# Kernel tuning notes

Measured on AMD Instinct MI355X. Metric: run time of the kernel, lower is better.

## Reference

```python
import jax, jax.numpy as jnp
import numpy as np

KH, KW = 2, 2
GRID_SIZE = 5
SPLINE_ORDER = 3
IN_FEATURES = KH * KW
N_COEF = GRID_SIZE + SPLINE_ORDER  # 8
N_KNOTS = GRID_SIZE + 2 * SPLINE_ORDER + 1  # 12


def b_splines(x, grid, spline_order):
    """x: (N, in), grid: (in, n_knots) -> (N, in, grid_size + spline_order).
    Cox-de-Boor recursion, identical to efficient-kan's b_splines."""
    x_ = x[..., None]  # (N, in, 1)
    bases = ((x_ >= grid[:, :-1]) & (x_ < grid[:, 1:])).astype(x.dtype)
    for k in range(1, spline_order + 1):
        left = (x_ - grid[:, : -(k + 1)]) / (grid[:, k:-1] - grid[:, : -(k + 1)])
        right = (grid[:, k + 1:] - x_) / (grid[:, k + 1:] - grid[:, 1:-k])
        bases = left * bases[..., :-1] + right * bases[..., 1:]
    return bases  # (N, in, N_COEF)


def setup_inputs() -> dict:
    key = jax.random.key(0)
    k1, k2, k3, k4 = jax.random.split(key, 4)
    B, C, H, W = 8, 16, 128, 128
    x = jax.random.normal(k1, (B, C, H, W), dtype=jnp.float32) * 0.5  # mostly inside grid_range
    base_weight = jax.random.normal(k2, (1, IN_FEATURES), dtype=jnp.float32) * 0.5
    spline_weight = jax.random.normal(k3, (1, IN_FEATURES, N_COEF), dtype=jnp.float32) * 0.1
    spline_scaler = 1.0 + jax.random.normal(k4, (1, IN_FEATURES), dtype=jnp.float32) * 0.1
    # uniform extended knot grid over grid_range=[-1, 1], same per input feature (buffer)
    h = 2.0 / GRID_SIZE
    g = np.arange(-SPLINE_ORDER, GRID_SIZE + SPLINE_ORDER + 1, dtype=np.float32) * h - 1.0
    grid = jnp.asarray(np.broadcast_to(g, (IN_FEATURES, N_KNOTS)).copy())
    return {"x": x, "base_weight": base_weight, "spline_weight": spline_weight,
            "spline_scaler": spline_scaler, "grid": grid}


def reference(x, base_weight, spline_weight, spline_scaler, grid):
    B, C, H, W = x.shape
    Ho, Wo = H - KH + 1, W - KW + 1  # stride 1, no padding, no dilation
    # unfold: (B, C, Ho, Wo, KH*KW), window elements in torch Unfold row-major order
    patches = jnp.stack([x[:, :, i:i + Ho, j:j + Wo]
                         for i in range(KH) for j in range(KW)], axis=-1)
    flat = patches.reshape(-1, IN_FEATURES)  # (N, 4)
    # KANLinear: base path (SiLU activation then linear)
    base = jax.nn.silu(flat) @ base_weight.T  # (N, 1)
    # spline path
    bas = b_splines(flat, grid, SPLINE_ORDER)  # (N, 4, 8)
    sw = spline_weight * spline_scaler[..., None]  # scaled_spline_weight (1, 4, 8)
    spline = bas.reshape(flat.shape[0], -1) @ sw.reshape(sw.shape[0], -1).T  # (N, 1)
    out = (base + spline).reshape(B, C, Ho, Wo)
    # multiple_convs_kan_conv2d accumulates the per-channel results into one output channel
    return out.sum(axis=1, keepdims=True)  # (B, 1, Ho, Wo)
```

## Files before the change

### kernel.cpp

```cpp
#include <hip/hip_runtime.h>


#define KH 2
#define KW 2
#define IN_F 4
#define N_COEF 8
#define N_INTERVALS 11

__device__ __forceinline__ float silu(float x) {
    return x * __builtin_amdgcn_rcpf(1.0f + __expf(-x));
}

__global__ __launch_bounds__(256) void kan_conv_kernel(
    const float* __restrict__ x,
    const float* __restrict__ base_w,
    const float* __restrict__ spline_w,
    const float* __restrict__ spline_s,
    const float* __restrict__ grid,
    float* __restrict__ out,
    int B, int C, int H, int W)
{
    const int Ho = H - 1, Wo = W - 1;

    __shared__ float4 coef[N_INTERVALS][IN_F];
    __shared__ float s_bw[IN_F];
    __shared__ float s_g0, s_invh;

    const int tid = threadIdx.x;
    if (tid < N_INTERVALS * IN_F) {
        const int t = tid / IN_F;
        const int p = tid % IN_F;
        const float M[4][4] = {
            {1.f/6.f, -3.f/6.f,  3.f/6.f, -1.f/6.f},
            {4.f/6.f,  0.f,     -6.f/6.f,  3.f/6.f},
            {1.f/6.f,  3.f/6.f,  3.f/6.f, -3.f/6.f},
            {0.f,      0.f,      0.f,      1.f/6.f}};
        const float scal = spline_s[p];
        float c0 = 0.f, c1 = 0.f, c2 = 0.f, c3 = 0.f;
        #pragma unroll
        for (int m = 0; m < 4; ++m) {
            const int j = t - 3 + m;
            const float w = (j >= 0 && j < N_COEF)
                              ? spline_w[p * N_COEF + j] * scal : 0.f;
            c0 += M[m][0] * w; c1 += M[m][1] * w;
            c2 += M[m][2] * w; c3 += M[m][3] * w;
        }
        coef[t][p] = make_float4(c0, c1, c2, c3);
    }
    if (tid < IN_F) s_bw[tid] = base_w[tid];
    if (tid == 0) { s_g0 = grid[0]; s_invh = 1.0f / (grid[1] - grid[0]); }
    __syncthreads();

    const float g0 = s_g0, invh = s_invh;
    const float bw0 = s_bw[0], bw1 = s_bw[1], bw2 = s_bw[2], bw3 = s_bw[3];

    const int total = B * Ho * Wo;
    const int HW = H * W;

    for (int o = blockIdx.x * blockDim.x + tid; o < total;
         o += gridDim.x * blockDim.x) {
        const int wo = o % Wo;
        const int rest = o / Wo;
        const int ho = rest % Ho;
        const int b = rest / Ho;

        const float* xb = x + (size_t)b * C * HW + (size_t)ho * W + wo;

        float acc = 0.f;
        #pragma unroll 4
        for (int c = 0; c < 16; ++c) {
            const float* xc = xb + (size_t)c * HW;
            const float v00 = xc[0];
            const float v01 = xc[1];
            const float v10 = xc[W];
            const float v11 = xc[W + 1];

            acc += silu(v00) * bw0 + silu(v01) * bw1 +
                   silu(v10) * bw2 + silu(v11) * bw3;

            #pragma unroll
            for (int p = 0; p < 4; ++p) {
                const float v = (p == 0) ? v00 : (p == 1) ? v01
                              : (p == 2) ? v10 : v11;
                const float tf = (v - g0) * invh;
                const float tfl = floorf(tf);
                const int ti = (int)tfl;
                if ((unsigned)ti < (unsigned)N_INTERVALS) {
                    const float u = tf - tfl;
                    const float4 cf = coef[ti][p];
                    float sp = fmaf(u, cf.w, cf.z);
                    sp = fmaf(u, sp, cf.y);
                    sp = fmaf(u, sp, cf.x);
                    acc += sp;
                }
            }
        }
        out[o] = acc;
    }
}

extern "C" void kernel_launch(void* const* d_in, const int* in_sizes, int n_in,
                              void* d_out, int out_size, void* d_ws, size_t ws_size,
                              hipStream_t stream) {
    const float* x        = (const float*)d_in[0];
    const float* base_w   = (const float*)d_in[1];
    const float* spline_w = (const float*)d_in[2];
    const float* spline_s = (const float*)d_in[3];
    const float* grid     = (const float*)d_in[4];
    float* out = (float*)d_out;

    const int B = 8, C = 16, H = 128, W = 128;
    const int total = B * (H - 1) * (W - 1);
    const int threads = 256;
    const int blocks = (total + threads - 1) / threads;

    kan_conv_kernel<<<blocks, threads, 0, stream>>>(
        x, base_w, spline_w, spline_s, grid, out, B, C, H, W);
}
```

Measured before the change: 75.58 us.

## Tile spatially with shared-memory per-pixel feature reuse and split channels across blocks

```diff
diff --git a/kernel.cpp b/kernel.cpp
--- a/kernel.cpp
+++ b/kernel.cpp
@@ -1,11 +1,15 @@
 #include <hip/hip_runtime.h>
 
 
-#define KH 2
-#define KW 2
 #define IN_F 4
 #define N_COEF 8
-#define N_INTERVALS 11
+#define N_INT 11
+#define TW 32
+#define TH 8
+#define LW 33
+#define LH 9
+#define NV (LW * LH)
+#define CG 4
 
 __device__ __forceinline__ float silu(float x) {
     return x * __builtin_amdgcn_rcpf(1.0f + __expf(-x));
@@ -22,12 +26,13 @@
 {
     const int Ho = H - 1, Wo = W - 1;
 
-    __shared__ float4 coef[N_INTERVALS][IN_F];
-    __shared__ float s_bw[IN_F];
-    __shared__ float s_g0, s_invh;
+    __shared__ float4 coef[N_INT][IN_F];
+    __shared__ float  sfeat[IN_F][NV];
+    __shared__ float  s_misc[6];
 
     const int tid = threadIdx.x;
-    if (tid < N_INTERVALS * IN_F) {
+
+    if (tid < N_INT * IN_F) {
         const int t = tid / IN_F;
         const int p = tid % IN_F;
         const float M[4][4] = {
@@ -47,56 +52,69 @@
         }
         coef[t][p] = make_float4(c0, c1, c2, c3);
     }
-    if (tid < IN_F) s_bw[tid] = base_w[tid];
-    if (tid == 0) { s_g0 = grid[0]; s_invh = 1.0f / (grid[1] - grid[0]); }
+    if (tid < IN_F) s_misc[tid] = base_w[tid];
+    if (tid == 4)   s_misc[4] = grid[0];
+    if (tid == 5)   s_misc[5] = 1.0f / (grid[1] - grid[0]);
+
+    int bid = blockIdx.x;
+    const int cg  = bid & 3;  bid >>= 2;
+    const int txi = bid & 3;  bid >>= 2;
+    const int tyi = bid & 15; bid >>= 4;
+    const int b   = bid;
+    const int tx0 = txi * TW, ty0 = tyi * TH, c0ch = cg * CG;
+
+    const int lx = tid & (TW - 1);
+    const int ly = tid >> 5;
+    const int oy = ty0 + ly, ox = tx0 + lx;
+
     __syncthreads();
+    const float bw0 = s_misc[0], bw1 = s_misc[1];
+    const float bw2 = s_misc[2], bw3 = s_misc[3];
+    const float g0 = s_misc[4], invh = s_misc[5];
+    const float bw[4] = {bw0, bw1, bw2, bw3};
 
-    const float g0 = s_g0, invh = s_invh;
-    const float bw0 = s_bw[0], bw1 = s_bw[1], bw2 = s_bw[2], bw3 = s_bw[3];
+    float acc = 0.f;
 
-    const int total = B * Ho * Wo;
-    const int HW = H * W;
+    #pragma unroll
+    for (int g = 0; g < CG; ++g) {
+        const int c = c0ch + g;
+        const float* __restrict__ xc = x + ((size_t)(b * C + c) * H) * W;
 
-    for (int o = blockIdx.x * blockDim.x + tid; o < total;
-         o += gridDim.x * blockDim.x) {
-        const int wo = o % Wo;
-        const int rest = o / Wo;
-        const int ho = rest % Ho;
-        const int b = rest / Ho;
+        if (g > 0) __syncthreads();
 
-        const float* xb = x + (size_t)b * C * HW + (size_t)ho * W + wo;
+        #pragma unroll
+        for (int v = tid; v < NV; v += 256) {
+            const int r  = v / LW;
+            const int cc = v - r * LW;
+            const int iy = ty0 + r, ix = tx0 + cc;
+            const float val = (iy < H && ix < W) ? xc[iy * W + ix] : 0.f;
 
-        float acc = 0.f;
-        #pragma unroll 4
-        for (int c = 0; c < 16; ++c) {
-            const float* xc = xb + (size_t)c * HW;
-            const float v00 = xc[0];
-            const float v01 = xc[1];
-            const float v10 = xc[W];
-            const float v11 = xc[W + 1];
-
-            acc += silu(v00) * bw0 + silu(v01) * bw1 +
-                   silu(v10) * bw2 + silu(v11) * bw3;
+            const float sil = silu(val);
+            const float tf  = (val - g0) * invh;
+            const float tfl = floorf(tf);
+            const int   ti  = (int)tfl;
+            const float u   = tf - tfl;
+            const bool  valid = ((unsigned)ti < (unsigned)N_INT);
+            const int   tc  = valid ? ti : 0;
 
             #pragma unroll
-            for (int p = 0; p < 4; ++p) {
-                const float v = (p == 0) ? v00 : (p == 1) ? v01
-                              : (p == 2) ? v10 : v11;
-                const float tf = (v - g0) * invh;
-                const float tfl = floorf(tf);
-                const int ti = (int)tfl;
-                if ((unsigned)ti < (unsigned)N_INTERVALS) {
-                    const float u = tf - tfl;
-                    const float4 cf = coef[ti][p];
-                    float sp = fmaf(u, cf.w, cf.z);
-                    sp = fmaf(u, sp, cf.y);
-                    sp = fmaf(u, sp, cf.x);
-                    acc += sp;
-                }
+            for (int p = 0; p < IN_F; ++p) {
+                const float4 cf = coef[tc][p];
+                float sp = fmaf(u, cf.w, cf.z);
+                sp = fmaf(u, sp, cf.y);
+                sp = fmaf(u, sp, cf.x);
+                sfeat[p][v] = fmaf(sil, bw[p], valid ? sp : 0.f);
             }
         }
-        out[o] = acc;
+        __syncthreads();
+
+        const int i00 = ly * LW + lx;
+        acc += sfeat[0][i00] + sfeat[1][i00 + 1]
+             + sfeat[2][i00 + LW] + sfeat[3][i00 + LW + 1];
     }
+
+    if (oy < Ho && ox < Wo)
+        atomicAdd(&out[((size_t)b * Ho + oy) * Wo + ox], acc);
 }
 
 extern "C" void kernel_launch(void* const* d_in, const int* in_sizes, int n_in,
@@ -110,10 +128,9 @@
     float* out = (float*)d_out;
 
     const int B = 8, C = 16, H = 128, W = 128;
-    const int total = B * (H - 1) * (W - 1);
-    const int threads = 256;
-    const int blocks = (total + threads - 1) / threads;
 
-    kan_conv_kernel<<<blocks, threads, 0, stream>>>(
+    hipMemsetAsync(out, 0, (size_t)out_size * sizeof(float), stream);
+
+    kan_conv_kernel<<<2048, 256, 0, stream>>>(
         x, base_w, spline_w, spline_s, grid, out, B, C, H, W);
 }
```

Measured after the change: 75.24 us. No clear change (-0.4%).
